# Optimization experiments

Measured on AMD Instinct MI355X. Metric: run time of the kernel, lower is better.

## Reference

```python
import jax, jax.numpy as jnp
import numpy as np

B, D, F, P = 65536, 256, 512, 256


def setup_inputs() -> dict:
    key = jax.random.key(0)
    k_x, k_f, k_p, k_a, k_b, k_t = jax.random.split(key, 6)
    x = jax.random.normal(k_x, (B, D), dtype=jnp.float32)
    # reset_parameters: uniform(-0.27, 1)
    features = jax.random.uniform(k_f, (F, D), dtype=jnp.float32, minval=-0.27, maxval=1.0)
    prototypes = jax.random.uniform(k_p, (P, D), dtype=jnp.float32, minval=-0.27, maxval=1.0)
    # alpha/beta/theta init to zeros in the module; use small random values so the
    # output is non-trivial for kernel correctness checking.
    alpha = jax.random.normal(k_a, (1,), dtype=jnp.float32) * 0.1
    beta = jax.random.normal(k_b, (1,), dtype=jnp.float32) * 0.1
    theta = jax.random.normal(k_t, (1,), dtype=jnp.float32) * 0.1
    return {"x": x, "features": features, "prototypes": prototypes,
            "alpha": alpha, "beta": beta, "theta": theta}


def reference(x, features, prototypes, alpha, beta, theta):
    # Shared projections
    x_features = x @ features.T                 # [B, F]
    p_features = prototypes @ features.T        # [P, F]
    x_present = jax.nn.relu(x_features)         # [B, F]
    p_present = jax.nn.relu(p_features)         # [P, F]
    x_weighted = x_features * x_present         # [B, F]
    p_weighted = p_features * p_present         # [P, F]

    # Tversky terms
    common = x_weighted @ p_weighted.T                          # [B, P]
    x_weighted_sum = jnp.sum(x_weighted, axis=1, keepdims=True)  # [B, 1]
    x_p_interaction = x_weighted @ p_present.T                  # [B, P]
    x_distinctive = x_weighted_sum - x_p_interaction            # [B, P]
    p_weighted_sum = jnp.sum(p_weighted, axis=1)[None, :]        # [1, P]
    x_p_weighted_interaction = x_present @ p_weighted.T         # [B, P]
    p_distinctive = p_weighted_sum - x_p_weighted_interaction   # [B, P]

    return theta * common - alpha * x_distinctive - beta * p_distinctive
```

## Files before the change

### kernel.cpp

```cpp
#include <hip/hip_runtime.h>
#include <cstdint>
#include <cstddef>

#define Bsz 65536
#define Dsz 256
#define Fsz 512
#define Psz 256

typedef __attribute__((ext_vector_type(8))) short short8;
typedef __attribute__((ext_vector_type(4))) short short4v;
typedef __attribute__((ext_vector_type(4))) float float4v;
typedef __attribute__((ext_vector_type(16))) float float16v;

__device__ inline short f2bf(float f) {
    unsigned u = __builtin_bit_cast(unsigned, f);
    u = (u + 0x7FFFu + ((u >> 16) & 1u)) >> 16;
    return (short)u;
}
__device__ inline float bf2f(short s) {
    unsigned u = ((unsigned)(unsigned short)s) << 16;
    return __builtin_bit_cast(float, u);
}


__global__ void k_prep(const float* __restrict__ features, short* __restrict__ featbB,
                       float* __restrict__ pws_neg) {
    int idx = blockIdx.x * 256 + threadIdx.x;
    int f = idx >> 5, d0 = (idx & 31) * 8;
    float4v v0 = *(const float4v*)(features + (size_t)f * Dsz + d0);
    float4v v1 = *(const float4v*)(features + (size_t)f * Dsz + d0 + 4);
    short8 s;
    s[0] = f2bf(v0.x); s[1] = f2bf(v0.y); s[2] = f2bf(v0.z); s[3] = f2bf(v0.w);
    s[4] = f2bf(v1.x); s[5] = f2bf(v1.y); s[6] = f2bf(v1.z); s[7] = f2bf(v1.w);
    int lane = (f & 15) + 16 * ((d0 >> 3) & 3);
    size_t o = (size_t)(f >> 4) * 4096 + (size_t)(d0 >> 5) * 512 + (size_t)lane * 8;
    *(short8*)&featbB[o] = s;
    if (idx < Psz) pws_neg[idx] = 0.f;
}

#define SBPITCH 136

__global__ __launch_bounds__(256, 2) void k_pside(
    const float* __restrict__ prototypes, const short* __restrict__ featbB,
    const float* __restrict__ beta_p,
    short* __restrict__ pwB, short* __restrict__ pmB, float* __restrict__ pws_neg)
{
    __shared__ char lds[35840];
    short* As = (short*)lds;
    short* Sb = (short*)lds;

    const int t = threadIdx.x;
    const int w = t >> 6, lane = t & 63, l15 = lane & 15, l4 = lane >> 4;
    const int rowg = blockIdx.x >> 2, nc = blockIdx.x & 3;
    const float beta = *beta_p;

    float4v acc[4][4];
    #pragma unroll
    for (int a = 0; a < 4; ++a)
        #pragma unroll
        for (int b = 0; b < 4; ++b) acc[a][b] = (float4v){0.f, 0.f, 0.f, 0.f};

    const float* pbase = prototypes + (size_t)rowg * 128 * Dsz;

    for (int kc = 0; kc < 4; ++kc) {
        __syncthreads();
        #pragma unroll
        for (int j = 0; j < 8; ++j) {
            int idx = j * 1024 + t * 4;
            int r = idx >> 6, c = idx & 63;
            float4v v = *(const float4v*)(pbase + (size_t)r * Dsz + kc * 64 + c);
            int unit = r * 8 + ((c >> 3) ^ (r & 7));
            short4v s; s.x = f2bf(v.x); s.y = f2bf(v.y); s.z = f2bf(v.z); s.w = f2bf(v.w);
            *(short4v*)((char*)As + unit * 16 + (c & 7) * 2) = s;
        }
        __syncthreads();
        #pragma unroll
        for (int kk = 0; kk < 2; ++kk) {
            short8 af[4], bf[4];
            const int k8 = kk * 4 + l4;
            #pragma unroll
            for (int tm = 0; tm < 4; ++tm) {
                int m = (w & 1) * 64 + tm * 16 + l15;
                af[tm] = *(const short8*)&As[(m * 8 + (k8 ^ (m & 7))) * 8];
            }
            #pragma unroll
            for (int tn = 0; tn < 4; ++tn) {
                int fcb = nc * 8 + (w >> 1) * 4 + tn;
                bf[tn] = *(const short8*)&featbB[(size_t)fcb * 4096 +
                                                 (size_t)(kc * 2 + kk) * 512 + (size_t)lane * 8];
            }
            #pragma unroll
            for (int tm = 0; tm < 4; ++tm)
                #pragma unroll
                for (int tn = 0; tn < 4; ++tn)
                    acc[tm][tn] = __builtin_amdgcn_mfma_f32_16x16x32_bf16(af[tm], bf[tn], acc[tm][tn], 0, 0, 0);
        }
    }
    __syncthreads();
    #pragma unroll
    for (int tm = 0; tm < 4; ++tm)
        #pragma unroll
        for (int tn = 0; tn < 4; ++tn)
            #pragma unroll
            for (int r = 0; r < 4; ++r) {
                int row = (w & 1) * 64 + tm * 16 + l4 * 4 + r;
                int col = (w >> 1) * 64 + tn * 16 + l15;
                Sb[row * SBPITCH + col] = f2bf(acc[tm][tn][r]);
            }
    __syncthreads();
    #pragma unroll
    for (int rep = 0; rep < 8; ++rep) {
        int u = rep * 256 + t;
        int row = u >> 4, i = u & 15;
        short8 sv = *(const short8*)&Sb[row * SBPITCH + i * 8];
        short8 pwv, pmv;
        float sum = 0.f;
        #pragma unroll
        for (int e = 0; e < 8; ++e) {
            float pf = bf2f(sv[e]);
            float pp = fmaxf(pf, 0.f);
            float pw = pf * pp;
            pwv[e] = f2bf(pw);
            pmv[e] = f2bf(pp - 1.0f);
            sum += pw;
        }
        int p = rowg * 128 + row;
        int gcol = nc * 128 + i * 8;
        size_t fo = (size_t)(gcol >> 4) * 4096 + (size_t)(p >> 5) * 512 +
                    (size_t)((p & 31) + 32 * ((gcol >> 3) & 1)) * 8;
        *(short8*)&pwB[fo] = pwv;
        *(short8*)&pmB[fo] = pmv;
        #pragma unroll
        for (int mk = 1; mk < 16; mk <<= 1) sum += __shfl_xor(sum, mk, 64);
        if ((lane & 15) == 0) atomicAdd(&pws_neg[p], -beta * sum);
    }
}

__global__ __launch_bounds__(256, 3) void k_main(
    const float* __restrict__ x, const short* __restrict__ featbB,
    const short* __restrict__ pwB, const short* __restrict__ pmB,
    const float* __restrict__ pws_neg,
    const float* __restrict__ alpha_p, const float* __restrict__ beta_p,
    const float* __restrict__ theta_p, float* __restrict__ out)
{
    __shared__ short A12[4096];

    const int t = threadIdx.x;
    const int w = t >> 6, lane = t & 63, l15 = lane & 15, l4 = lane >> 4;
    const int l31 = lane & 31, half = lane >> 5;
    const int rowg = blockIdx.x >> 1, ch = blockIdx.x & 1;
    const int ntile = ch * 4 + w;
    const float alpha = *alpha_p, beta = *beta_p, theta = *theta_p;
    const size_t row0 = (size_t)rowg * 64;

    short8 xreg[8];
    {
        const float* xr = x + (row0 + 16 * w + l15) * Dsz + l4 * 8;
        #pragma unroll
        for (int kk = 0; kk < 8; ++kk) {
            float4v v0 = *(const float4v*)(xr + kk * 32);
            float4v v1 = *(const float4v*)(xr + kk * 32 + 4);
            short8 s;
            s[0] = f2bf(v0.x); s[1] = f2bf(v0.y); s[2] = f2bf(v0.z); s[3] = f2bf(v0.w);
            s[4] = f2bf(v1.x); s[5] = f2bf(v1.y); s[6] = f2bf(v1.z); s[7] = f2bf(v1.w);
            xreg[kk] = s;
        }
    }

    float16v acc[2];
    #pragma unroll
    for (int a = 0; a < 2; ++a)
        #pragma unroll
        for (int e = 0; e < 16; ++e) acc[a][e] = 0.f;

    const int mbase = 16 * w + l4 * 4;
    const size_t lane8 = (size_t)lane * 8;

    short8 fbA[8], fbB[8], pA[2], pB[2];

    #pragma unroll
    for (int kk = 0; kk < 8; ++kk)
        fbA[kk] = *(const short8*)(featbB + kk * 512 + lane8);
    pA[0] = *(const short8*)(pwB + (size_t)ntile * 512 + lane8);
    pA[1] = *(const short8*)(pmB + (size_t)ntile * 512 + lane8);

    auto body = [&](int fc, short8 (&fbc)[8], short8 (&fbn)[8],
                    short8 (&pc)[2], short8 (&pn)[2]) {
        const int buf = (fc & 1) << 11;
        const int fcn = (fc + 1) & 31;
        const short* fbsrc = featbB + (size_t)fcn * 4096 + lane8;

        float4v s0 = (float4v){0.f, 0.f, 0.f, 0.f};
        float4v s1 = (float4v){0.f, 0.f, 0.f, 0.f};
        #pragma unroll
        for (int kk = 0; kk < 8; kk += 2) {
            s0 = __builtin_amdgcn_mfma_f32_16x16x32_bf16(xreg[kk],     fbc[kk],     s0, 0, 0, 0);
            s1 = __builtin_amdgcn_mfma_f32_16x16x32_bf16(xreg[kk + 1], fbc[kk + 1], s1, 0, 0, 0);
        }

        #pragma unroll
        for (int kk = 0; kk < 4; ++kk) fbn[kk] = *(const short8*)(fbsrc + kk * 512);
        pn[0] = *(const short8*)(pwB + (size_t)fcn * 4096 + (size_t)ntile * 512 + lane8);
        pn[1] = *(const short8*)(pmB + (size_t)fcn * 4096 + (size_t)ntile * 512 + lane8);

        #pragma unroll
        for (int r = 0; r < 4; ++r) {
            float sv = s0[r] + s1[r];
            float xp = fmaxf(sv, 0.f);
            float xw = sv * xp;
            int m = mbase + r;
            int swz = (m >> 2) & 3;
            A12[buf + (m * 4 + ((l15 >> 3) ^ swz)) * 8 + (l15 & 7)]       = f2bf(theta * xw + beta * xp);
            A12[buf + (m * 4 + ((2 | (l15 >> 3)) ^ swz)) * 8 + (l15 & 7)] = f2bf(alpha * xw);
        }
        __syncthreads();

        #pragma unroll
        for (int kk = 4; kk < 8; ++kk) fbn[kk] = *(const short8*)(fbsrc + kk * 512);

        #pragma unroll
        for (int mi = 0; mi < 2; ++mi) {
            int m = 32 * mi + l31;
            int swz = (m >> 2) & 3;
            short8 a1 = *(const short8*)&A12[buf + (m * 4 + (half ^ swz)) * 8];
            short8 a2 = *(const short8*)&A12[buf + (m * 4 + ((2 | half) ^ swz)) * 8];
            acc[mi] = __builtin_amdgcn_mfma_f32_32x32x16_bf16(a1, pc[0], acc[mi], 0, 0, 0);
            acc[mi] = __builtin_amdgcn_mfma_f32_32x32x16_bf16(a2, pc[1], acc[mi], 0, 0, 0);
        }
    };

    #pragma unroll 1
    for (int fc = 0; fc < 32; fc += 2) {
        body(fc,     fbA, fbB, pA, pB);
        body(fc + 1, fbB, fbA, pB, pA);
    }

    {
        int col = ntile * 32 + l31;
        float pn_ = pws_neg[col];
        #pragma unroll
        for (int mi = 0; mi < 2; ++mi)
            #pragma unroll
            for (int rg = 0; rg < 16; ++rg) {
                size_t grow = row0 + 32 * mi + (rg & 3) + 8 * (rg >> 2) + 4 * half;
                out[grow * Psz + col] = acc[mi][rg] + pn_;
            }
    }
}

extern "C" void kernel_launch(void* const* d_in, const int* in_sizes, int n_in,
                              void* d_out, int out_size, void* d_ws, size_t ws_size,
                              hipStream_t stream) {
    const float* x          = (const float*)d_in[0];
    const float* features   = (const float*)d_in[1];
    const float* prototypes = (const float*)d_in[2];
    const float* alpha      = (const float*)d_in[3];
    const float* beta       = (const float*)d_in[4];
    const float* theta      = (const float*)d_in[5];
    float* out = (float*)d_out;

    char* ws = (char*)d_ws;
    short* featbB  = (short*)(ws);
    short* pwB     = (short*)(ws + 262144);
    short* pmB     = (short*)(ws + 524288);
    float* pws_neg = (float*)(ws + 786432);

    hipLaunchKernelGGL(k_prep,  dim3(64),   dim3(256), 0, stream, features, featbB, pws_neg);
    hipLaunchKernelGGL(k_pside, dim3(8),    dim3(256), 0, stream, prototypes, featbB, beta,
                       pwB, pmB, pws_neg);
    hipLaunchKernelGGL(k_main,  dim3(2048), dim3(256), 0, stream, x, featbB, pwB, pmB,
                       pws_neg, alpha, beta, theta, out);
}
```

Before: 223.2 us.

## Cover all prototype columns per block to avoid recomputing x projection twice

Each block now handles 64 rows against all 256 prototypes (each wave takes two 32-column tiles) instead of splitting the columns across two blocks. This halves the redundant first-stage x@features MFMA work, the x loads and the bf16 conversion per row, and halves the grid. In exchange each wave holds twice the accumulators and prototype fragments, so launch bounds drop to 2 blocks per CU. The next-chunk feature prefetch is also hoisted to the start of each iteration.

After: 193.8 us. 1.15x faster.

```diff
diff --git a/kernel.cpp b/kernel.cpp
--- a/kernel.cpp
+++ b/kernel.cpp
@@ -136,7 +136,7 @@
     }
 }
 
-__global__ __launch_bounds__(256, 3) void k_main(
+__global__ __launch_bounds__(256, 2) void k_main(
     const float* __restrict__ x, const short* __restrict__ featbB,
     const short* __restrict__ pwB, const short* __restrict__ pmB,
     const float* __restrict__ pws_neg,
@@ -148,10 +148,8 @@
     const int t = threadIdx.x;
     const int w = t >> 6, lane = t & 63, l15 = lane & 15, l4 = lane >> 4;
     const int l31 = lane & 31, half = lane >> 5;
-    const int rowg = blockIdx.x >> 1, ch = blockIdx.x & 1;
-    const int ntile = ch * 4 + w;
     const float alpha = *alpha_p, beta = *beta_p, theta = *theta_p;
-    const size_t row0 = (size_t)rowg * 64;
+    const size_t row0 = (size_t)blockIdx.x * 64;
 
     short8 xreg[8];
     {
@@ -167,41 +165,49 @@
         }
     }
 
-    float16v acc[2];
+    float16v acc[2][2];
     #pragma unroll
     for (int a = 0; a < 2; ++a)
         #pragma unroll
-        for (int e = 0; e < 16; ++e) acc[a][e] = 0.f;
+        for (int b = 0; b < 2; ++b)
+            #pragma unroll
+            for (int e = 0; e < 16; ++e) acc[a][b][e] = 0.f;
 
     const int mbase = 16 * w + l4 * 4;
     const size_t lane8 = (size_t)lane * 8;
-
-    short8 fbA[8], fbB[8], pA[2], pB[2];
+    const size_t pwoff = (size_t)w * 1024 + lane8;
+
+    short8 fbR[2][8];
+    short8 pR[2][4];
 
     #pragma unroll
     for (int kk = 0; kk < 8; ++kk)
-        fbA[kk] = *(const short8*)(featbB + kk * 512 + lane8);
-    pA[0] = *(const short8*)(pwB + (size_t)ntile * 512 + lane8);
-    pA[1] = *(const short8*)(pmB + (size_t)ntile * 512 + lane8);
-
-    auto body = [&](int fc, short8 (&fbc)[8], short8 (&fbn)[8],
-                    short8 (&pc)[2], short8 (&pn)[2]) {
+        fbR[0][kk] = *(const short8*)(featbB + kk * 512 + lane8);
+    pR[0][0] = *(const short8*)(pwB + pwoff);
+    pR[0][1] = *(const short8*)(pwB + pwoff + 512);
+    pR[0][2] = *(const short8*)(pmB + pwoff);
+    pR[0][3] = *(const short8*)(pmB + pwoff + 512);
+
+    auto body = [&](int fc, int cur, int nxt) {
         const int buf = (fc & 1) << 11;
         const int fcn = (fc + 1) & 31;
+
         const short* fbsrc = featbB + (size_t)fcn * 4096 + lane8;
+        #pragma unroll
+        for (int kk = 0; kk < 8; ++kk)
+            fbR[nxt][kk] = *(const short8*)(fbsrc + kk * 512);
+        pR[nxt][0] = *(const short8*)(pwB + (size_t)fcn * 4096 + pwoff);
+        pR[nxt][1] = *(const short8*)(pwB + (size_t)fcn * 4096 + pwoff + 512);
+        pR[nxt][2] = *(const short8*)(pmB + (size_t)fcn * 4096 + pwoff);
+        pR[nxt][3] = *(const short8*)(pmB + (size_t)fcn * 4096 + pwoff + 512);
 
         float4v s0 = (float4v){0.f, 0.f, 0.f, 0.f};
         float4v s1 = (float4v){0.f, 0.f, 0.f, 0.f};
         #pragma unroll
         for (int kk = 0; kk < 8; kk += 2) {
-            s0 = __builtin_amdgcn_mfma_f32_16x16x32_bf16(xreg[kk],     fbc[kk],     s0, 0, 0, 0);
-            s1 = __builtin_amdgcn_mfma_f32_16x16x32_bf16(xreg[kk + 1], fbc[kk + 1], s1, 0, 0, 0);
-        }
-
-        #pragma unroll
-        for (int kk = 0; kk < 4; ++kk) fbn[kk] = *(const short8*)(fbsrc + kk * 512);
-        pn[0] = *(const short8*)(pwB + (size_t)fcn * 4096 + (size_t)ntile * 512 + lane8);
-        pn[1] = *(const short8*)(pmB + (size_t)fcn * 4096 + (size_t)ntile * 512 + lane8);
+            s0 = __builtin_amdgcn_mfma_f32_16x16x32_bf16(xreg[kk],     fbR[cur][kk],     s0, 0, 0, 0);
+            s1 = __builtin_amdgcn_mfma_f32_16x16x32_bf16(xreg[kk + 1], fbR[cur][kk + 1], s1, 0, 0, 0);
+        }
 
         #pragma unroll
         for (int r = 0; r < 4; ++r) {
@@ -216,34 +222,34 @@
         __syncthreads();
 
         #pragma unroll
-        for (int kk = 4; kk < 8; ++kk) fbn[kk] = *(const short8*)(fbsrc + kk * 512);
-
-        #pragma unroll
         for (int mi = 0; mi < 2; ++mi) {
             int m = 32 * mi + l31;
             int swz = (m >> 2) & 3;
             short8 a1 = *(const short8*)&A12[buf + (m * 4 + (half ^ swz)) * 8];
             short8 a2 = *(const short8*)&A12[buf + (m * 4 + ((2 | half) ^ swz)) * 8];
-            acc[mi] = __builtin_amdgcn_mfma_f32_32x32x16_bf16(a1, pc[0], acc[mi], 0, 0, 0);
-            acc[mi] = __builtin_amdgcn_mfma_f32_32x32x16_bf16(a2, pc[1], acc[mi], 0, 0, 0);
+            acc[mi][0] = __builtin_amdgcn_mfma_f32_32x32x16_bf16(a1, pR[cur][0], acc[mi][0], 0, 0, 0);
+            acc[mi][0] = __builtin_amdgcn_mfma_f32_32x32x16_bf16(a2, pR[cur][2], acc[mi][0], 0, 0, 0);
+            acc[mi][1] = __builtin_amdgcn_mfma_f32_32x32x16_bf16(a1, pR[cur][1], acc[mi][1], 0, 0, 0);
+            acc[mi][1] = __builtin_amdgcn_mfma_f32_32x32x16_bf16(a2, pR[cur][3], acc[mi][1], 0, 0, 0);
         }
     };
 
     #pragma unroll 1
     for (int fc = 0; fc < 32; fc += 2) {
-        body(fc,     fbA, fbB, pA, pB);
-        body(fc + 1, fbB, fbA, pB, pA);
-    }
-
-    {
-        int col = ntile * 32 + l31;
+        body(fc,     0, 1);
+        body(fc + 1, 1, 0);
+    }
+
+    #pragma unroll
+    for (int ni = 0; ni < 2; ++ni) {
+        int col = 64 * w + 32 * ni + l31;
         float pn_ = pws_neg[col];
         #pragma unroll
         for (int mi = 0; mi < 2; ++mi)
             #pragma unroll
             for (int rg = 0; rg < 16; ++rg) {
                 size_t grow = row0 + 32 * mi + (rg & 3) + 8 * (rg >> 2) + 4 * half;
-                out[grow * Psz + col] = acc[mi][rg] + pn_;
+                out[grow * Psz + col] = acc[mi][ni][rg] + pn_;
             }
     }
 }
@@ -268,6 +274,6 @@
     hipLaunchKernelGGL(k_prep,  dim3(64),   dim3(256), 0, stream, features, featbB, pws_neg);
     hipLaunchKernelGGL(k_pside, dim3(8),    dim3(256), 0, stream, prototypes, featbB, beta,
                        pwB, pmB, pws_neg);
-    hipLaunchKernelGGL(k_main,  dim3(2048), dim3(256), 0, stream, x, featbB, pwB, pmB,
+    hipLaunchKernelGGL(k_main,  dim3(1024), dim3(256), 0, stream, x, featbB, pwB, pmB,
                        pws_neg, alpha, beta, theta, out);
 }
```
